# Optimization experiments

Measured on AMD Instinct MI355X. Metric: run time of the kernel, lower is better.

The kernel has to match this reference:

```python
import jax, jax.numpy as jnp
import numpy as np

B, S, DIM, H = 2, 2048, 1024, 16
DH = DIM // H            # 64
G = DH // 4              # 16 quaternion groups per head
IQ = DIM // 4            # 256
ROPE_BASE = 10000.0
SCALE = DH ** -0.5


def qlinear(x, wr, wi, wj, wk, b):
    # x: [B,S,4*IQ]; strided quaternion components, exact combo from QuaternionLinear.forward
    xr, xi, xj, xk = x[..., 0::4], x[..., 1::4], x[..., 2::4], x[..., 3::4]
    o_r = xr @ wr.T - xi @ wi.T - xj @ wj.T - xk @ wk.T
    o_i = xi @ wr.T + xr @ wi.T + xk @ wk.T - xj @ wj.T
    o_j = xj @ wr.T - xk @ wk.T + xr @ wj.T + xi @ wi.T
    o_k = xk @ wr.T + xj @ wj.T - xi @ wi.T + xr @ wk.T
    out = jnp.stack([o_r, o_i, o_j, o_k], axis=-1).reshape(x.shape[:-1] + (-1,))
    return out + b


def qrope(x):
    # x: [B,H,S,DH]; left quaternion multiply u(theta) \otimes q, axis_mode='cycle'
    b, h, s, dh = x.shape
    g = dh // 4
    xq = x.reshape(b, h, s, g, 4)
    t = jnp.arange(s, dtype=x.dtype)
    inv = 1.0 / (ROPE_BASE ** (jnp.arange(g, dtype=x.dtype) / g))
    ang = t[:, None] * inv[None, :]            # [S,G]
    cos, sin = jnp.cos(ang), jnp.sin(ang)
    gi = jnp.arange(g)
    ax_i = (gi % 3 == 0).astype(x.dtype)
    ax_j = (gi % 3 == 1).astype(x.dtype)
    ax_k = (gi % 3 == 2).astype(x.dtype)
    ur, ui, uj, uk = cos, sin * ax_i, sin * ax_j, sin * ax_k   # [S,G] broadcast over [B,H,S,G]
    xr, xi, xj, xk = xq[..., 0], xq[..., 1], xq[..., 2], xq[..., 3]
    pr = ur * xr - ui * xi - uj * xj - uk * xk
    pi = ur * xi + ui * xr + uj * xk - uk * xj
    pj = ur * xj - ui * xk + uj * xr + uk * xi
    pk = ur * xk + ui * xj - uj * xi + uk * xr
    return jnp.stack([pr, pi, pj, pk], axis=-1).reshape(b, h, s, dh)


def setup_inputs() -> dict:
    key = jax.random.key(0)
    ks = jax.random.split(key, 24)
    x = jax.random.normal(ks[0], (B, S, DIM), dtype=jnp.float32)
    # causal mask: True = masked
    mask = jnp.broadcast_to(jnp.triu(jnp.ones((S, S), dtype=bool), k=1), (B, S, S))
    inp = {"x": x, "mask": mask}
    i = 1
    for proj in ("q", "k", "v", "o"):
        for comp in ("wr", "wi", "wj", "wk"):
            inp[f"{proj}_{comp}"] = jax.random.normal(ks[i], (IQ, IQ), dtype=jnp.float32) * 0.02
            i += 1
        inp[f"{proj}_b"] = jnp.zeros((DIM,), dtype=jnp.float32)
    return inp


def reference(x, mask,
              q_wr, q_wi, q_wj, q_wk, q_b,
              k_wr, k_wi, k_wj, k_wk, k_b,
              v_wr, v_wi, v_wj, v_wk, v_b,
              o_wr, o_wi, o_wj, o_wk, o_b):
    b, s, dm = x.shape
    q = qlinear(x, q_wr, q_wi, q_wj, q_wk, q_b).reshape(b, s, H, DH).transpose(0, 2, 1, 3)
    k = qlinear(x, k_wr, k_wi, k_wj, k_wk, k_b).reshape(b, s, H, DH).transpose(0, 2, 1, 3)
    v = qlinear(x, v_wr, v_wi, v_wj, v_wk, v_b).reshape(b, s, H, DH).transpose(0, 2, 1, 3)
    q, k = qrope(q), qrope(k)
    scores = jnp.einsum('bhsd,bhtd->bhst', q, k) * SCALE
    scores = jnp.where(mask[:, None, :, :], -jnp.inf, scores)
    a = jax.nn.softmax(scores, axis=-1)
    out = jnp.einsum('bhst,bhtd->bhsd', a, v).transpose(0, 2, 1, 3).reshape(b, s, dm)
    return qlinear(out, o_wr, o_wi, o_wj, o_wk, o_b)
```

## Files before the change

### kernel.cpp

```cpp
#include <hip/hip_runtime.h>
#include <stdint.h>

typedef unsigned short u16;
typedef unsigned int   u32;

#define NB   2
#define NS   2048
#define NDIM 1024
#define NH   16
#define NDH  64
#define QSCALE 0.18033688011112042f

typedef __bf16 bf16x8 __attribute__((ext_vector_type(8)));
typedef float  f32x4  __attribute__((ext_vector_type(4)));

#define MFMA_BF16(a,b,c) __builtin_amdgcn_mfma_f32_16x16x32_bf16((a),(b),(c),0,0,0)

#define XBF_OFF   (256)
#define WD_OFF    (XBF_OFF  + 8*1024*1024)
#define BIAS_OFF  (WD_OFF   + 8*1024*1024)
#define QB_OFF    (BIAS_OFF + 16384)
#define KB_OFF    (QB_OFF   + 8*1024*1024)
#define VT_OFF    (KB_OFF   + 8*1024*1024)
#define OP_OFF    (VT_OFF   + 8*1024*1024)
#define LP_OFF    (OP_OFF   + 16*1024*1024)

__device__ __forceinline__ float bf2f(u16 h){
  union { u32 u; float f; } v; v.u = ((u32)h) << 16; return v.f;
}
__device__ __forceinline__ u16 f2bf(float f){
  union { float f; u32 u; } v; v.f = f;
  u32 r = (v.u >> 16) & 1u;
  return (u16)((v.u + 0x7fffu + r) >> 16);
}
__device__ __forceinline__ float load_val(const void* p, int i, int isbf){
  return isbf ? bf2f(((const u16*)p)[i]) : ((const float*)p)[i];
}
__device__ __forceinline__ void gl_lds16(const u16* g, u16* l){
  __builtin_amdgcn_global_load_lds(
      (__attribute__((address_space(1))) void*)(uintptr_t)g,
      (__attribute__((address_space(3))) void*)(uintptr_t)l,
      16, 0, 0);
}

__global__ void detect_kernel(const u16* __restrict__ x, int* __restrict__ flag){
  __shared__ int cnt;
  if (threadIdx.x == 0) cnt = 0;
  __syncthreads();
  int ok = 0;
  int base = threadIdx.x * 16;
  for (int i = base; i < base + 16; ++i){
    u16 h = x[i];
    int e = (h >> 7) & 0xFF;
    if ((e > 96 && e < 158) || ((h & 0x7FFF) == 0)) ok++;
  }
  atomicAdd(&cnt, ok);
  __syncthreads();
  if (threadIdx.x == 0) *flag = (cnt > 3600) ? 1 : 0;
}

__global__ void conv_x_kernel(const void* __restrict__ xin, u16* __restrict__ xbf,
                              const int* __restrict__ flag){
  int isbf = *flag;
  int t = blockIdx.x * 256 + threadIdx.x;
  if (isbf){
    ((uint4*)xbf)[t] = ((const uint4*)xin)[t];
  } else {
    const float4* f4 = (const float4*)xin;
    float4 a = f4[2*t], b = f4[2*t+1];
    ushort4 lo = { f2bf(a.x), f2bf(a.y), f2bf(a.z), f2bf(a.w) };
    ushort4 hi = { f2bf(b.x), f2bf(b.y), f2bf(b.z), f2bf(b.w) };
    ((ushort4*)xbf)[2*t]   = lo;
    ((ushort4*)xbf)[2*t+1] = hi;
  }
}

struct QPtrs { const void* w[16]; const void* b[4]; };

__global__ void build_w_kernel(QPtrs ptrs, u16* __restrict__ wd,
                               float* __restrict__ biasf, const int* __restrict__ flag){
  int isbf = *flag;
  int idx = blockIdx.x * 256 + threadIdx.x;
  int n = idx & 255, m = (idx >> 8) & 255, c = (idx >> 16) & 3, p = idx >> 18;
  int src = m * 256 + n;
  float vr = load_val(ptrs.w[p*4+0], src, isbf);
  float vi = load_val(ptrs.w[p*4+1], src, isbf);
  float vj = load_val(ptrs.w[p*4+2], src, isbf);
  float vk = load_val(ptrs.w[p*4+3], src, isbf);
  float o0, o1, o2, o3;
  switch (c){
    case 0:  o0 = vr; o1 = -vi; o2 = -vj; o3 = -vk; break;
    case 1:  o0 = vi; o1 =  vr; o2 = -vj; o3 =  vk; break;
    case 2:  o0 = vj; o1 =  vi; o2 =  vr; o3 = -vk; break;
    default: o0 = vk; o1 = -vi; o2 =  vj; o3 =  vr; break;
  }
  ushort4 sv = { f2bf(o0), f2bf(o1), f2bf(o2), f2bf(o3) };
  *(ushort4*)&wd[(size_t)p * 1048576 + (size_t)(4*m + c) * 1024 + 4*n] = sv;
  if (idx < 4096){
    int pp = idx >> 10, oo = idx & 1023;
    biasf[idx] = load_val(ptrs.b[pp], oo, isbf);
  }
}

__global__ __launch_bounds__(256)
void gemm_qkv_kernel(const u16* __restrict__ A, const u16* __restrict__ Bw,
                     const float* __restrict__ bias,
                     u16* __restrict__ qb, u16* __restrict__ kb, u16* __restrict__ vt){
  __shared__ u16 sA[128 * 32];
  __shared__ u16 sB[128 * 32];
  int tid = threadIdx.x, w = tid >> 6, lane = tid & 63, quad = lane >> 4, l16 = lane & 15;
  int n0 = blockIdx.x * 128, m0 = blockIdx.y * 128;

  f32x4 acc[4][4];
#pragma unroll
  for (int i = 0; i < 4; ++i)
#pragma unroll
    for (int j = 0; j < 4; ++j) acc[i][j] = (f32x4){0.f, 0.f, 0.f, 0.f};

  int eo = w * 512 + lane * 8;
  int r0 = eo >> 5, c0 = eo & 31;
  const u16* ga = A  + (size_t)(m0 + r0) * 1024 + c0;
  const u16* gb = Bw + (size_t)(n0 + r0) * 1024 + c0;
  u16* la = &sA[eo];
  u16* lb = &sB[eo];
  int mw = (w & 1) * 64, nw = (w >> 1) * 64;

  for (int k0 = 0; k0 < 1024; k0 += 32){
#pragma unroll
    for (int i = 0; i < 2; ++i){
      gl_lds16(ga + (size_t)i * 65536 + k0, la + i * 2048);
      gl_lds16(gb + (size_t)i * 65536 + k0, lb + i * 2048);
    }
    __syncthreads();
    bf16x8 af[4], bfr[4];
#pragma unroll
    for (int mt = 0; mt < 4; ++mt)
      af[mt] = *(const bf16x8*)&sA[(mw + mt*16 + l16) * 32 + quad * 8];
#pragma unroll
    for (int nt = 0; nt < 4; ++nt)
      bfr[nt] = *(const bf16x8*)&sB[(nw + nt*16 + l16) * 32 + quad * 8];
#pragma unroll
    for (int mt = 0; mt < 4; ++mt)
#pragma unroll
      for (int nt = 0; nt < 4; ++nt)
        acc[mt][nt] = MFMA_BF16(af[mt], bfr[nt], acc[mt][nt]);
    __syncthreads();
  }

#pragma unroll
  for (int mt = 0; mt < 4; ++mt){
    int row = m0 + mw + mt*16 + quad*4;
    int b = row >> 11, seq0 = row & 2047;
#pragma unroll
    for (int nt = 0; nt < 4; ++nt){
      int col = n0 + nw + nt*16 + l16;
      int proj = col >> 10, o = col & 1023;
      int h = o >> 6, d = o & 63;
      float bv = bias[col];
      if (proj == 2){
        ushort4 pv = { f2bf(acc[mt][nt][0] + bv), f2bf(acc[mt][nt][1] + bv),
                       f2bf(acc[mt][nt][2] + bv), f2bf(acc[mt][nt][3] + bv) };
        *(ushort4*)&vt[((size_t)((b*16 + h) * 64 + d)) * 2048 + seq0] = pv;
      } else {
        u16* dst = proj ? kb : qb;
#pragma unroll
        for (int r = 0; r < 4; ++r)
          dst[((size_t)((b*16 + h) * 2048 + seq0 + r)) * 64 + d] = f2bf(acc[mt][nt][r] + bv);
      }
    }
  }
}

__global__ __launch_bounds__(256)
void gemm_o_kernel(const u16* __restrict__ A, const u16* __restrict__ Bw,
                   const float* __restrict__ bias, void* __restrict__ dout,
                   const int* __restrict__ flag){
  __shared__ u16 sA[64 * 32];
  __shared__ u16 sB[128 * 32];
  int tid = threadIdx.x, w = tid >> 6, lane = tid & 63, quad = lane >> 4, l16 = lane & 15;
  int n0 = blockIdx.x * 128, m0 = blockIdx.y * 64;

  f32x4 acc[2][4];
#pragma unroll
  for (int i = 0; i < 2; ++i)
#pragma unroll
    for (int j = 0; j < 4; ++j) acc[i][j] = (f32x4){0.f, 0.f, 0.f, 0.f};

  int mw = (w & 1) * 32, nw = (w >> 1) * 64;

  for (int k0 = 0; k0 < 1024; k0 += 32){
#pragma unroll
    for (int i = 0; i < 3; ++i){
      int c = w * 3 + i;
      int eo = (c < 4 ? c : c - 4) * 512 + lane * 8;
      int r0 = eo >> 5, c0 = eo & 31;
      if (c < 4) gl_lds16(A  + (size_t)(m0 + r0) * 1024 + k0 + c0, &sA[eo]);
      else       gl_lds16(Bw + (size_t)(n0 + r0) * 1024 + k0 + c0, &sB[eo]);
    }
    __syncthreads();
    bf16x8 af[2], bfr[4];
#pragma unroll
    for (int mt = 0; mt < 2; ++mt)
      af[mt] = *(const bf16x8*)&sA[(mw + mt*16 + l16) * 32 + quad * 8];
#pragma unroll
    for (int nt = 0; nt < 4; ++nt)
      bfr[nt] = *(const bf16x8*)&sB[(nw + nt*16 + l16) * 32 + quad * 8];
#pragma unroll
    for (int mt = 0; mt < 2; ++mt)
#pragma unroll
      for (int nt = 0; nt < 4; ++nt)
        acc[mt][nt] = MFMA_BF16(af[mt], bfr[nt], acc[mt][nt]);
    __syncthreads();
  }

  int isbf = *flag;
#pragma unroll
  for (int mt = 0; mt < 2; ++mt){
    int row = m0 + mw + mt*16 + quad*4;
#pragma unroll
    for (int nt = 0; nt < 4; ++nt){
      int col = n0 + nw + nt*16 + l16;
      float bv = bias[col];
#pragma unroll
      for (int r = 0; r < 4; ++r){
        float val = acc[mt][nt][r] + bv;
        size_t addr = (size_t)(row + r) * 1024 + col;
        if (isbf) ((u16*)dout)[addr] = f2bf(val);
        else      ((float*)dout)[addr] = val;
      }
    }
  }
}

__global__ void rope_kernel(u16* __restrict__ qb, u16* __restrict__ kb){
  int idx = blockIdx.x * 256 + threadIdx.x;
  int which = idx >> 20;
  int r = idx & 1048575;
  u16* buf = which ? kb : qb;
  int g = r & 15, s = (r >> 4) & 2047, bh = r >> 15;
  size_t base = ((size_t)bh * 2048 + s) * 64 + g * 4;
  ushort4 xv = *(ushort4*)&buf[base];
  float xr = bf2f(xv.x), xi = bf2f(xv.y), xj = bf2f(xv.z), xk = bf2f(xv.w);
  float inv = __builtin_amdgcn_exp2f(-(float)g * 0.8304820237218405f);
  float ang = (float)s * inv;
  float co = __cosf(ang), si = __sinf(ang);
  float sc = which ? 1.0f : QSCALE;
  co *= sc; si *= sc;
  int ax = g % 3;
  float ui = (ax == 0) ? si : 0.f;
  float uj = (ax == 1) ? si : 0.f;
  float uk = (ax == 2) ? si : 0.f;
  float pr = co*xr - ui*xi - uj*xj - uk*xk;
  float pi = co*xi + ui*xr + uj*xk - uk*xj;
  float pj = co*xj - ui*xk + uj*xr + uk*xi;
  float pk = co*xk + ui*xj - uj*xi + uk*xr;
  ushort4 res = { f2bf(pr), f2bf(pi), f2bf(pj), f2bf(pk) };
  *(ushort4*)&buf[base] = res;
}

#define SPT 20

__global__ __launch_bounds__(256, 3)
void attn_kernel(const u16* __restrict__ Q, const u16* __restrict__ K,
                 const u16* __restrict__ Vt, u16* __restrict__ OP,
                 float* __restrict__ LP){
  __shared__ u16 sK[2][4096];
  __shared__ u16 sPT[4][64 * SPT];
  int bh  = blockIdx.x;
  int spl = blockIdx.y;
  int qt  = 15 - (int)blockIdx.z;
  int tid = threadIdx.x, w = tid >> 6, lane = tid & 63, quad = lane >> 4, l16 = lane & 15;
  size_t kbase = (size_t)bh * 2048 * 64;
  size_t vbase = (size_t)bh * 64 * 2048;
  int rowbase = qt * 128 + w * 32;
  u16* spw = &sPT[w][0];

  bf16x8 qf[2][2];
#pragma unroll
  for (int g = 0; g < 2; ++g)
#pragma unroll
    for (int kc = 0; kc < 2; ++kc)
      qf[g][kc] = *(const bf16x8*)(Q + kbase + (size_t)(rowbase + g*16 + l16) * 64 + kc*32 + quad*8);

  f32x4 oaccT[2][4];
  float lsum[2][4];
#pragma unroll
  for (int g = 0; g < 2; ++g)
#pragma unroll
    for (int i = 0; i < 4; ++i){ oaccT[g][i] = (f32x4){0.f,0.f,0.f,0.f}; lsum[g][i] = 0.f; }

  int kt0 = spl ? (qt + 1) : 0;
  int ntiles = qt + 1;

  auto stage = [&](int kt, int b){
    int kcol = kt * 64;
#pragma unroll
    for (int p = 0; p < 2; ++p){
      int slot = w*128 + p*64 + lane;
      int row = slot >> 3, dc = (slot & 7) ^ (row & 7);
      gl_lds16(K + kbase + (size_t)(kcol + row) * 64 + dc*8, &sK[b][(w*128 + p*64) * 8]);
    }
  };

  stage(kt0, 0);
  for (int i = 0; i < ntiles; ++i){
    int kcol = (kt0 + i) * 64;
    __syncthreads();
    if (i + 1 < ntiles) stage(kt0 + i + 1, (i + 1) & 1);
    const u16* bK = sK[i & 1];

    if (kcol <= rowbase + 31){
      bf16x8 vf[4][2];
#pragma unroll
      for (int dn = 0; dn < 4; ++dn)
#pragma unroll
        for (int kc = 0; kc < 2; ++kc)
          vf[dn][kc] = *(const bf16x8*)(Vt + vbase + (size_t)(dn*16 + l16) * 2048
                                        + kcol + kc*32 + quad*8);
      bf16x8 bk[2][4];
#pragma unroll
      for (int kc = 0; kc < 2; ++kc)
#pragma unroll
        for (int nt = 0; nt < 4; ++nt){
          int rw = nt*16 + l16;
          int ch = ((kc*4 + quad) ^ (rw & 7)) * 8;
          bk[kc][nt] = *(const bf16x8*)&bK[rw*64 + ch];
        }
#pragma unroll
      for (int g = 0; g < 2; ++g){
        int G0 = rowbase + g*16;
        if (kcol <= G0 + 15){
          f32x4 sacc[4];
#pragma unroll
          for (int nt = 0; nt < 4; ++nt) sacc[nt] = (f32x4){0.f,0.f,0.f,0.f};
#pragma unroll
          for (int kc = 0; kc < 2; ++kc)
#pragma unroll
            for (int nt = 0; nt < 4; ++nt)
              sacc[nt] = MFMA_BF16(qf[g][kc], bk[kc][nt], sacc[nt]);

          if (kcol + 63 > G0){
#pragma unroll
            for (int nt = 0; nt < 4; ++nt){
              int col = kcol + nt*16 + l16;
              ushort4 pv;
#pragma unroll
              for (int r = 0; r < 4; ++r){
                int row = G0 + quad*4 + r;
                float pp = (col <= row) ? __builtin_amdgcn_exp2f(sacc[nt][r]) : 0.f;
                lsum[g][r] += pp;
                ((u16*)&pv)[r] = f2bf(pp);
              }
              *(ushort4*)&spw[(nt*16 + l16) * SPT + quad*4] = pv;
            }
          } else {
#pragma unroll
            for (int nt = 0; nt < 4; ++nt){
              ushort4 pv;
#pragma unroll
              for (int r = 0; r < 4; ++r){
                float pp = __builtin_amdgcn_exp2f(sacc[nt][r]);
                lsum[g][r] += pp;
                ((u16*)&pv)[r] = f2bf(pp);
              }
              *(ushort4*)&spw[(nt*16 + l16) * SPT + quad*4] = pv;
            }
          }
#pragma unroll
          for (int kc = 0; kc < 2; ++kc){
            bf16x8 pf;
#pragma unroll
            for (int j = 0; j < 8; ++j)
              pf[j] = ((const __bf16*)spw)[(kc*32 + quad*8 + j) * SPT + l16];
#pragma unroll
            for (int dn = 0; dn < 4; ++dn)
              oaccT[g][dn] = MFMA_BF16(vf[dn][kc], pf, oaccT[g][dn]);
          }
        }
      }
    }
  }

  float* scr = (float*)spw;
#pragma unroll
  for (int g = 0; g < 2; ++g)
#pragma unroll
    for (int r = 0; r < 4; ++r){
      float l = lsum[g][r];
      l += __shfl_xor(l, 1); l += __shfl_xor(l, 2);
      l += __shfl_xor(l, 4); l += __shfl_xor(l, 8);
      if (l16 == 0) scr[g*16 + quad*4 + r] = l;
    }
  float lrow[2];
#pragma unroll
  for (int g = 0; g < 2; ++g) lrow[g] = scr[g*16 + l16];

  size_t obase = ((size_t)(spl*32 + bh)) * 2048;
#pragma unroll
  for (int g = 0; g < 2; ++g){
    int row = rowbase + g*16 + l16;
    if (quad == 0) LP[obase + row] = lrow[g];
#pragma unroll
    for (int dn = 0; dn < 4; ++dn){
      ushort4 ov = { f2bf(oaccT[g][dn][0]), f2bf(oaccT[g][dn][1]),
                     f2bf(oaccT[g][dn][2]), f2bf(oaccT[g][dn][3]) };
      *(ushort4*)&OP[(obase + row) * 64 + dn*16 + quad*4] = ov;
    }
  }
}

__global__ void combine_kernel(const u16* __restrict__ OP, const float* __restrict__ LP,
                               u16* __restrict__ Ab){
  int idx = blockIdx.x * 256 + threadIdx.x;
  int dc = idx & 7, s = (idx >> 3) & 2047, bh = idx >> 14;
  size_t r0 = (size_t)bh * 2048 + s, r1 = (size_t)(32 + bh) * 2048 + s;
  float invl = 1.f / (LP[r0] + LP[r1]);
  union { uint4 v; u16 h[8]; } a0, a1; ushort4 o[2];
  a0.v = *(const uint4*)&OP[r0 * 64 + dc*8];
  a1.v = *(const uint4*)&OP[r1 * 64 + dc*8];
#pragma unroll
  for (int p = 0; p < 2; ++p)
#pragma unroll
    for (int j = 0; j < 4; ++j)
      ((u16*)&o[p])[j] = f2bf((bf2f(a0.h[p*4+j]) + bf2f(a1.h[p*4+j])) * invl);
  int b = bh >> 4, h = bh & 15;
  u16* dst = &Ab[((size_t)(b*2048 + s)) * 1024 + h*64 + dc*8];
  *(ushort4*)dst = o[0];
  *(ushort4*)(dst + 4) = o[1];
}

extern "C" void kernel_launch(void* const* d_in, const int* in_sizes, int n_in,
                              void* d_out, int out_size, void* d_ws, size_t ws_size,
                              hipStream_t stream){
  (void)in_sizes; (void)n_in; (void)out_size; (void)ws_size;
  char* ws = (char*)d_ws;
  int*   flag  = (int*)ws;
  u16*   Xbf   = (u16*)(ws + XBF_OFF);
  u16*   Wd    = (u16*)(ws + WD_OFF);
  float* biasf = (float*)(ws + BIAS_OFF);
  u16*   Qb    = (u16*)(ws + QB_OFF);
  u16*   Kb    = (u16*)(ws + KB_OFF);
  u16*   Vt    = (u16*)(ws + VT_OFF);
  u16*   OP    = (u16*)(ws + OP_OFF);
  float* LP    = (float*)(ws + LP_OFF);
  u16*   Ab    = Xbf;

  detect_kernel<<<1, 256, 0, stream>>>((const u16*)d_in[0], flag);
  conv_x_kernel<<<2048, 256, 0, stream>>>(d_in[0], Xbf, flag);

  QPtrs ptrs;
  for (int p = 0; p < 4; ++p){
    for (int wi = 0; wi < 4; ++wi) ptrs.w[p*4 + wi] = d_in[2 + p*5 + wi];
    ptrs.b[p] = d_in[2 + p*5 + 4];
  }
  build_w_kernel<<<4096, 256, 0, stream>>>(ptrs, Wd, biasf, flag);

  gemm_qkv_kernel<<<dim3(24, 32), 256, 0, stream>>>(Xbf, Wd, biasf, Qb, Kb, Vt);
  rope_kernel<<<8192, 256, 0, stream>>>(Qb, Kb);
  attn_kernel<<<dim3(32, 2, 16), 256, 0, stream>>>(Qb, Kb, Vt, OP, LP);
  combine_kernel<<<2048, 256, 0, stream>>>(OP, LP, Ab);
  gemm_o_kernel<<<dim3(8, 64), 256, 0, stream>>>(Ab, Wd + 3*1048576, biasf + 3072,
                                                 d_out, flag);
}
```

Before: 262.0 us.

## Fuse quaternion RoPE into QKV GEMM epilogue and double-buffer GEMM LDS

Applies the quaternion rotary embedding and the Q scale inside the QKV GEMM epilogue, using a lane shuffle to fetch the partner component, and removes the separate rope kernel along with its read-modify-write pass over Q and K. Both GEMMs now double-buffer their LDS tiles so the next k-slice loads while the current one computes, leaving one barrier per iteration. An XOR swizzle on the LDS column is added to reduce bank conflicts. The cost is more LDS per block and more transcendental work in the epilogue, which may lower occupancy.

Result: faster. 254.3 us (-2.9%).

```diff
diff --git a/kernel.cpp b/kernel.cpp
--- a/kernel.cpp
+++ b/kernel.cpp
@@ -106,8 +106,8 @@
 void gemm_qkv_kernel(const u16* __restrict__ A, const u16* __restrict__ Bw,
                      const float* __restrict__ bias,
                      u16* __restrict__ qb, u16* __restrict__ kb, u16* __restrict__ vt){
-  __shared__ u16 sA[128 * 32];
-  __shared__ u16 sB[128 * 32];
+  __shared__ u16 sA[2][128 * 32];
+  __shared__ u16 sB[2][128 * 32];
   int tid = threadIdx.x, w = tid >> 6, lane = tid & 63, quad = lane >> 4, l16 = lane & 15;
   int n0 = blockIdx.x * 128, m0 = blockIdx.y * 128;
 
@@ -117,55 +117,87 @@
 #pragma unroll
     for (int j = 0; j < 4; ++j) acc[i][j] = (f32x4){0.f, 0.f, 0.f, 0.f};
 
-  int eo = w * 512 + lane * 8;
-  int r0 = eo >> 5, c0 = eo & 31;
-  const u16* ga = A  + (size_t)(m0 + r0) * 1024 + c0;
-  const u16* gb = Bw + (size_t)(n0 + r0) * 1024 + c0;
-  u16* la = &sA[eo];
-  u16* lb = &sB[eo];
+  int cp = lane & 3, rl = lane >> 2;
+  int gc = (cp ^ ((rl >> 1) & 3)) * 8;
+  const u16* ga = A  + (size_t)(m0 + w*16 + rl) * 1024 + gc;
+  const u16* gb = Bw + (size_t)(n0 + w*16 + rl) * 1024 + gc;
+  int ldo = w * 512 + lane * 8;
+  int xorv = ((l16 >> 1) & 3) * 8;
   int mw = (w & 1) * 64, nw = (w >> 1) * 64;
 
-  for (int k0 = 0; k0 < 1024; k0 += 32){
+  auto stage = [&](int k0, int b){
 #pragma unroll
     for (int i = 0; i < 2; ++i){
-      gl_lds16(ga + (size_t)i * 65536 + k0, la + i * 2048);
-      gl_lds16(gb + (size_t)i * 65536 + k0, lb + i * 2048);
-    }
+      gl_lds16(ga + (size_t)i * 65536 + k0, &sA[b][ldo + i * 2048]);
+      gl_lds16(gb + (size_t)i * 65536 + k0, &sB[b][ldo + i * 2048]);
+    }
+  };
+
+  stage(0, 0);
+  for (int it = 0; it < 32; ++it){
     __syncthreads();
+    if (it < 31) stage((it + 1) * 32, (it + 1) & 1);
+    const u16* cA = sA[it & 1];
+    const u16* cB = sB[it & 1];
     bf16x8 af[4], bfr[4];
 #pragma unroll
     for (int mt = 0; mt < 4; ++mt)
-      af[mt] = *(const bf16x8*)&sA[(mw + mt*16 + l16) * 32 + quad * 8];
+      af[mt] = *(const bf16x8*)&cA[(mw + mt*16 + l16) * 32 + (quad*8 ^ xorv)];
 #pragma unroll
     for (int nt = 0; nt < 4; ++nt)
-      bfr[nt] = *(const bf16x8*)&sB[(nw + nt*16 + l16) * 32 + quad * 8];
+      bfr[nt] = *(const bf16x8*)&cB[(nw + nt*16 + l16) * 32 + (quad*8 ^ xorv)];
 #pragma unroll
     for (int mt = 0; mt < 4; ++mt)
 #pragma unroll
       for (int nt = 0; nt < 4; ++nt)
         acc[mt][nt] = MFMA_BF16(af[mt], bfr[nt], acc[mt][nt]);
-    __syncthreads();
-  }
-
-#pragma unroll
-  for (int mt = 0; mt < 4; ++mt){
-    int row = m0 + mw + mt*16 + quad*4;
-    int b = row >> 11, seq0 = row & 2047;
-#pragma unroll
-    for (int nt = 0; nt < 4; ++nt){
-      int col = n0 + nw + nt*16 + l16;
-      int proj = col >> 10, o = col & 1023;
-      int h = o >> 6, d = o & 63;
-      float bv = bias[col];
-      if (proj == 2){
+  }
+
+  int proj = n0 >> 10;
+  if (proj == 2){
+#pragma unroll
+    for (int mt = 0; mt < 4; ++mt){
+      int row = m0 + mw + mt*16 + quad*4;
+      int b = row >> 11, seq0 = row & 2047;
+#pragma unroll
+      for (int nt = 0; nt < 4; ++nt){
+        int col = n0 + nw + nt*16 + l16;
+        int o = col & 1023, h = o >> 6, d = o & 63;
+        float bv = bias[col];
         ushort4 pv = { f2bf(acc[mt][nt][0] + bv), f2bf(acc[mt][nt][1] + bv),
                        f2bf(acc[mt][nt][2] + bv), f2bf(acc[mt][nt][3] + bv) };
         *(ushort4*)&vt[((size_t)((b*16 + h) * 64 + d)) * 2048 + seq0] = pv;
-      } else {
-        u16* dst = proj ? kb : qb;
-#pragma unroll
-        for (int r = 0; r < 4; ++r)
-          dst[((size_t)((b*16 + h) * 2048 + seq0 + r)) * 64 + d] = f2bf(acc[mt][nt][r] + bv);
+      }
+    }
+  } else {
+    float sc = (proj == 0) ? QSCALE : 1.0f;
+    u16* dst = proj ? kb : qb;
+    int c = l16 & 3;
+#pragma unroll
+    for (int nt = 0; nt < 4; ++nt){
+      int col = n0 + nw + nt*16 + l16;
+      int o = col & 1023, h = o >> 6, d = o & 63;
+      int g = d >> 2;
+      int ax = g % 3;
+      int mask = ax + 1;
+      int tbl = (ax == 0) ? 0xA : (ax == 1 ? 0x6 : 0xC);
+      float sgn = ((tbl >> c) & 1) ? 1.f : -1.f;
+      float inv = __builtin_amdgcn_exp2f(-(float)g * 0.8304820237218405f);
+      float bv = bias[col];
+#pragma unroll
+      for (int mt = 0; mt < 4; ++mt){
+        int row0 = m0 + mw + mt*16 + quad*4;
+        int b = row0 >> 11, s0 = row0 & 2047;
+        size_t obase = ((size_t)((b*16 + h) * 2048 + s0)) * 64 + d;
+#pragma unroll
+        for (int r = 0; r < 4; ++r){
+          float v = acc[mt][nt][r] + bv;
+          float vp = __shfl_xor(v, mask);
+          float ang = (float)(s0 + r) * inv;
+          float co = __cosf(ang) * sc;
+          float si = __sinf(ang) * sc * sgn;
+          dst[obase + (size_t)r * 64] = f2bf(co * v + si * vp);
+        }
       }
     }
   }
@@ -175,8 +207,8 @@
 void gemm_o_kernel(const u16* __restrict__ A, const u16* __restrict__ Bw,
                    const float* __restrict__ bias, void* __restrict__ dout,
                    const int* __restrict__ flag){
-  __shared__ u16 sA[64 * 32];
-  __shared__ u16 sB[128 * 32];
+  __shared__ u16 sA[2][64 * 32];
+  __shared__ u16 sB[2][128 * 32];
   int tid = threadIdx.x, w = tid >> 6, lane = tid & 63, quad = lane >> 4, l16 = lane & 15;
   int n0 = blockIdx.x * 128, m0 = blockIdx.y * 64;
 
@@ -186,31 +218,40 @@
 #pragma unroll
     for (int j = 0; j < 4; ++j) acc[i][j] = (f32x4){0.f, 0.f, 0.f, 0.f};
 
+  int cp = lane & 3, rl = lane >> 2;
+  int gc = (cp ^ ((rl >> 1) & 3)) * 8;
+  int xorv = ((l16 >> 1) & 3) * 8;
   int mw = (w & 1) * 32, nw = (w >> 1) * 64;
 
-  for (int k0 = 0; k0 < 1024; k0 += 32){
+  auto stage = [&](int k0, int b){
 #pragma unroll
     for (int i = 0; i < 3; ++i){
-      int c = w * 3 + i;
-      int eo = (c < 4 ? c : c - 4) * 512 + lane * 8;
-      int r0 = eo >> 5, c0 = eo & 31;
-      if (c < 4) gl_lds16(A  + (size_t)(m0 + r0) * 1024 + k0 + c0, &sA[eo]);
-      else       gl_lds16(Bw + (size_t)(n0 + r0) * 1024 + k0 + c0, &sB[eo]);
-    }
+      int ch = w * 3 + i;
+      int lr = (ch < 4 ? ch : ch - 4) * 16 + rl;
+      int eo = (ch < 4 ? ch : ch - 4) * 512 + lane * 8;
+      if (ch < 4) gl_lds16(A  + (size_t)(m0 + lr) * 1024 + k0 + gc, &sA[b][eo]);
+      else        gl_lds16(Bw + (size_t)(n0 + lr) * 1024 + k0 + gc, &sB[b][eo]);
+    }
+  };
+
+  stage(0, 0);
+  for (int it = 0; it < 32; ++it){
     __syncthreads();
+    if (it < 31) stage((it + 1) * 32, (it + 1) & 1);
+    const u16* cA = sA[it & 1];
+    const u16* cB = sB[it & 1];
     bf16x8 af[2], bfr[4];
 #pragma unroll
     for (int mt = 0; mt < 2; ++mt)
-      af[mt] = *(const bf16x8*)&sA[(mw + mt*16 + l16) * 32 + quad * 8];
+      af[mt] = *(const bf16x8*)&cA[(mw + mt*16 + l16) * 32 + (quad*8 ^ xorv)];
 #pragma unroll
     for (int nt = 0; nt < 4; ++nt)
-      bfr[nt] = *(const bf16x8*)&sB[(nw + nt*16 + l16) * 32 + quad * 8];
+      bfr[nt] = *(const bf16x8*)&cB[(nw + nt*16 + l16) * 32 + (quad*8 ^ xorv)];
 #pragma unroll
     for (int mt = 0; mt < 2; ++mt)
 #pragma unroll
       for (int nt = 0; nt < 4; ++nt)
         acc[mt][nt] = MFMA_BF16(af[mt], bfr[nt], acc[mt][nt]);
-    __syncthreads();
   }
 
   int isbf = *flag;
@@ -230,32 +271,6 @@
       }
     }
   }
-}
-
-__global__ void rope_kernel(u16* __restrict__ qb, u16* __restrict__ kb){
-  int idx = blockIdx.x * 256 + threadIdx.x;
-  int which = idx >> 20;
-  int r = idx & 1048575;
-  u16* buf = which ? kb : qb;
-  int g = r & 15, s = (r >> 4) & 2047, bh = r >> 15;
-  size_t base = ((size_t)bh * 2048 + s) * 64 + g * 4;
-  ushort4 xv = *(ushort4*)&buf[base];
-  float xr = bf2f(xv.x), xi = bf2f(xv.y), xj = bf2f(xv.z), xk = bf2f(xv.w);
-  float inv = __builtin_amdgcn_exp2f(-(float)g * 0.8304820237218405f);
-  float ang = (float)s * inv;
-  float co = __cosf(ang), si = __sinf(ang);
-  float sc = which ? 1.0f : QSCALE;
-  co *= sc; si *= sc;
-  int ax = g % 3;
-  float ui = (ax == 0) ? si : 0.f;
-  float uj = (ax == 1) ? si : 0.f;
-  float uk = (ax == 2) ? si : 0.f;
-  float pr = co*xr - ui*xi - uj*xj - uk*xk;
-  float pi = co*xi + ui*xr + uj*xk - uk*xj;
-  float pj = co*xj - ui*xk + uj*xr + uk*xi;
-  float pk = co*xk + ui*xj - uj*xi + uk*xr;
-  ushort4 res = { f2bf(pr), f2bf(pi), f2bf(pj), f2bf(pk) };
-  *(ushort4*)&buf[base] = res;
 }
 
 #define SPT 20
@@ -456,7 +471,6 @@
   build_w_kernel<<<4096, 256, 0, stream>>>(ptrs, Wd, biasf, flag);
 
   gemm_qkv_kernel<<<dim3(24, 32), 256, 0, stream>>>(Xbf, Wd, biasf, Qb, Kb, Vt);
-  rope_kernel<<<8192, 256, 0, stream>>>(Qb, Kb);
   attn_kernel<<<dim3(32, 2, 16), 256, 0, stream>>>(Qb, Kb, Vt, OP, LP);
   combine_kernel<<<2048, 256, 0, stream>>>(OP, LP, Ab);
   gemm_o_kernel<<<dim3(8, 64), 256, 0, stream>>>(Ab, Wd + 3*1048576, biasf + 3072,
```
